# Kernel optimization log

Measured on AMD Instinct MI355X. Metric: run time of the kernel, lower is better.

The kernel has to match this reference:

```python
import jax, jax.numpy as jnp
import numpy as np

NUM_BINS = 64
BIN_WIDTH = 0.0625
X_SHAPE = (64, 4, 512, 512)  # SD-style latent batch, ~268 MB fp32


def setup_inputs() -> dict:
    key = jax.random.key(0)
    x = jax.random.normal(key, X_SHAPE, dtype=jnp.float32)
    # uniform bin centers over [-2, 2), step = BIN_WIDTH (matches init_kwargs)
    bins = (-2.0 + BIN_WIDTH * jnp.arange(NUM_BINS)).astype(jnp.float32)
    bin_width = jnp.float32(BIN_WIDTH)
    return {"x": x, "bins": bins, "bin_width": bin_width}


def reference(x, bins, bin_width):
    # out[b] = mean(0.5 - 0.5 * tanh((x - bins[b]) / bin_width * 2))
    # lax.map over the small fixed bin axis avoids materializing a
    # [num_bins, *x.shape] intermediate, matching the original's per-bin
    # streaming reduction.
    scale = 2.0 / bin_width

    def per_bin(c):
        return jnp.mean(0.5 - 0.5 * jnp.tanh((x - c) * scale))

    return jax.lax.map(per_bin, bins)  # shape [NUM_BINS]
```

## Files before the change

### kernel.cpp

```cpp
#include <hip/hip_runtime.h>


#define NCELLS   (74 * 64)
#define NBINS    64
#define NGROUPS  74
#define HIST_BLOCKS  2048
#define HIST_THREADS 256

typedef float floatv4 __attribute__((ext_vector_type(4)));

__global__ void __launch_bounds__(HIST_THREADS, 8)
hist_fold_kernel(const float* __restrict__ x,
                 double* __restrict__ part, int n)
{
    __shared__ unsigned hist[NCELLS];
    __shared__ unsigned G[NGROUPS];
    __shared__ unsigned P[NBINS];

    const int tid = threadIdx.x;

    for (int i = tid; i < NCELLS; i += HIST_THREADS) hist[i] = 0u;
    __syncthreads();

    const int n4 = n >> 2;
    const floatv4* __restrict__ x4 = (const floatv4*)x;
    const int stride = HIST_BLOCKS * HIST_THREADS;
    int i = blockIdx.x * HIST_THREADS + tid;

#define BUMP1(val) do {                                   \
        int f = (int)fmaf((val), 1024.0f, 2368.0f);       \
        f = min(max(f, 0), NCELLS - 1);                   \
        atomicAdd(&hist[f], 1u);                          \
    } while (0)
#define BUMP4(v) do { BUMP1((v).x); BUMP1((v).y); BUMP1((v).z); BUMP1((v).w); } while (0)

    bool have = (i + 3 * stride < n4);
    floatv4 c0, c1, c2, c3;
    if (have) {
        c0 = x4[i]; c1 = x4[i + stride]; c2 = x4[i + 2 * stride]; c3 = x4[i + 3 * stride];
    }
    while (have) {
        const int j = i + 4 * stride;
        const bool nhave = (j + 3 * stride < n4);
        floatv4 n0, n1, n2, n3;
        if (nhave) {
            n0 = x4[j]; n1 = x4[j + stride]; n2 = x4[j + 2 * stride]; n3 = x4[j + 3 * stride];
        }
        BUMP4(c0); BUMP4(c1); BUMP4(c2); BUMP4(c3);
        c0 = n0; c1 = n1; c2 = n2; c3 = n3;
        i = j; have = nhave;
    }
    for (; i < n4; i += stride) {
        floatv4 a = x4[i];
        BUMP4(a);
    }
    if (blockIdx.x == 0) {
        int tail = n & 3;
        if (tid < tail) { float v = x[(n4 << 2) + tid]; BUMP1(v); }
    }
    __syncthreads();

    const int wave = tid >> 6;
    const int lane = tid & 63;

    float sig_r[10];
    #pragma unroll
    for (int p = 0; p < 10; ++p) {
        float z = (319.5f - (float)((p << 6) + lane)) * 0.0625f;
        sig_r[p] = 1.0f / (1.0f + __expf(-z));
    }

    for (int g = wave; g < NGROUPS; g += HIST_THREADS / 64) {
        unsigned v = hist[(g << 6) + lane];
        #pragma unroll
        for (int o = 32; o; o >>= 1) v += __shfl_xor(v, o);
        if (lane == 0) G[g] = v;
    }
    __syncthreads();

    if (tid < NBINS) {
        unsigned p = 0;
        for (int g = 0; g < tid; ++g) p += G[g];
        P[tid] = p;
    }
    __syncthreads();

    #pragma unroll
    for (int bi = 0; bi < 16; ++bi) {
        const int b = (wave << 4) + bi;
        float ws = 0.0f;
        const int base = (b << 6) + lane;
        #pragma unroll
        for (int p = 0; p < 10; ++p)
            ws += (float)hist[base + (p << 6)] * sig_r[p];
        #pragma unroll
        for (int o = 32; o; o >>= 1) ws += __shfl_xor(ws, o);
        if (lane == 0)
            part[(b << 11) + blockIdx.x] = (double)P[b] + (double)ws;
    }
#undef BUMP1
#undef BUMP4
}

__global__ void __launch_bounds__(256)
finalize_kernel(const double* __restrict__ part,
                float* __restrict__ out, double invN)
{
    const int b = blockIdx.x;
    const int tid = threadIdx.x;
    double s = 0.0;
    for (int j = tid; j < HIST_BLOCKS; j += 256)
        s += part[(b << 11) + j];
    __shared__ double sd[256];
    sd[tid] = s;
    __syncthreads();
    for (int ofs = 128; ofs > 0; ofs >>= 1) {
        if (tid < ofs) sd[tid] += sd[tid + ofs];
        __syncthreads();
    }
    if (tid == 0) out[b] = (float)(sd[0] * invN);
}

extern "C" void kernel_launch(void* const* d_in, const int* in_sizes, int n_in,
                              void* d_out, int out_size, void* d_ws, size_t ws_size,
                              hipStream_t stream)
{
    const float* x = (const float*)d_in[0];
    const int n = in_sizes[0];
    double* part = (double*)d_ws;

    hist_fold_kernel<<<HIST_BLOCKS, HIST_THREADS, 0, stream>>>(x, part, n);
    finalize_kernel<<<NBINS, 256, 0, stream>>>(part, (float*)d_out,
                                               1.0 / (double)n);
}
```

Measured before the change: 377.8 us.

## Assign contiguous chunks per wave with triple-buffered register prefetch

```diff
diff --git a/kernel.cpp b/kernel.cpp
--- a/kernel.cpp
+++ b/kernel.cpp
@@ -6,6 +6,8 @@
 #define NGROUPS  74
 #define HIST_BLOCKS  2048
 #define HIST_THREADS 256
+#define F4_PER_WAVE  2048
+#define NWAVES   (HIST_BLOCKS * HIST_THREADS / 64)
 
 typedef float floatv4 __attribute__((ext_vector_type(4)));
 
@@ -24,8 +26,8 @@
 
     const int n4 = n >> 2;
     const floatv4* __restrict__ x4 = (const floatv4*)x;
-    const int stride = HIST_BLOCKS * HIST_THREADS;
-    int i = blockIdx.x * HIST_THREADS + tid;
+    const int lane  = tid & 63;
+    const int gwave = ((blockIdx.x * HIST_THREADS) + tid) >> 6;
 
 #define BUMP1(val) do {                                   \
         int f = (int)fmaf((val), 1024.0f, 2368.0f);       \
@@ -34,25 +36,30 @@
     } while (0)
 #define BUMP4(v) do { BUMP1((v).x); BUMP1((v).y); BUMP1((v).z); BUMP1((v).w); } while (0)
 
-    bool have = (i + 3 * stride < n4);
-    floatv4 c0, c1, c2, c3;
-    if (have) {
-        c0 = x4[i]; c1 = x4[i + stride]; c2 = x4[i + 2 * stride]; c3 = x4[i + 3 * stride];
-    }
-    while (have) {
-        const int j = i + 4 * stride;
-        const bool nhave = (j + 3 * stride < n4);
-        floatv4 n0, n1, n2, n3;
-        if (nhave) {
-            n0 = x4[j]; n1 = x4[j + stride]; n2 = x4[j + 2 * stride]; n3 = x4[j + 3 * stride];
+    for (int base = gwave * F4_PER_WAVE; base < n4; base += NWAVES * F4_PER_WAVE) {
+        if (base + F4_PER_WAVE <= n4) {
+            const floatv4* __restrict__ p = x4 + base + lane;
+            floatv4 A0,A1,A2,A3, B0,B1,B2,B3, C0,C1,C2,C3;
+#define ISSUE(S, g) do { S##0 = p[(g)*256]; S##1 = p[(g)*256+64]; \
+                         S##2 = p[(g)*256+128]; S##3 = p[(g)*256+192]; } while (0)
+#define CONSUME(S) do { BUMP4(S##0); BUMP4(S##1); BUMP4(S##2); BUMP4(S##3); } while (0)
+            ISSUE(A, 0); ISSUE(B, 1); ISSUE(C, 2);
+            CONSUME(A); ISSUE(A, 3);
+            CONSUME(B); ISSUE(B, 4);
+            CONSUME(C); ISSUE(C, 5);
+            CONSUME(A); ISSUE(A, 6);
+            CONSUME(B); ISSUE(B, 7);
+            CONSUME(C);
+            CONSUME(A);
+            CONSUME(B);
+#undef ISSUE
+#undef CONSUME
+        } else {
+            for (int q = lane; q < F4_PER_WAVE; q += 64) {
+                int idx = base + q;
+                if (idx < n4) { floatv4 v = x4[idx]; BUMP4(v); }
+            }
         }
-        BUMP4(c0); BUMP4(c1); BUMP4(c2); BUMP4(c3);
-        c0 = n0; c1 = n1; c2 = n2; c3 = n3;
-        i = j; have = nhave;
-    }
-    for (; i < n4; i += stride) {
-        floatv4 a = x4[i];
-        BUMP4(a);
     }
     if (blockIdx.x == 0) {
         int tail = n & 3;
@@ -61,7 +68,6 @@
     __syncthreads();
 
     const int wave = tid >> 6;
-    const int lane = tid & 63;
 
     float sig_r[10];
     #pragma unroll
@@ -89,10 +95,10 @@
     for (int bi = 0; bi < 16; ++bi) {
         const int b = (wave << 4) + bi;
         float ws = 0.0f;
-        const int base = (b << 6) + lane;
+        const int cbase = (b << 6) + lane;
         #pragma unroll
         for (int p = 0; p < 10; ++p)
-            ws += (float)hist[base + (p << 6)] * sig_r[p];
+            ws += (float)hist[cbase + (p << 6)] * sig_r[p];
         #pragma unroll
         for (int o = 32; o; o >>= 1) ws += __shfl_xor(ws, o);
         if (lane == 0)
```

Result: faster. 368.2 us (-2.5%).
